# Kernel optimization log

Measured on AMD Instinct MI355X. Metric: run time of the kernel, lower is better.

Reference implementation:

```python
import jax, jax.numpy as jnp
import numpy as np

HIDDEN = [256, 128, 64, 32]
N_IN, N_OUT = 784, 10
V_REST = 0.0; V_RESET = 0.0; V_TH = 1.0; R_MEM = 1.0; DT = 1.0; TAU = 2.0
ALPHA = DT / TAU
SLOPE = 5.0
B, T = 128, 500


def setup_inputs() -> dict:
    key = jax.random.key(0)
    ks = jax.random.split(key, 7)
    sizes = [N_IN] + HIDDEN + [N_OUT]
    inp = {"input_spikes": jax.random.uniform(ks[0], (B, N_IN, T), dtype=jnp.float32)}
    for i in range(len(sizes) - 1):  # 5 weight matrices
        inp[f"w{i}"] = jax.random.uniform(ks[i + 1], (sizes[i], sizes[i + 1]), dtype=jnp.float32) * 0.1
    return inp


def _lif(v, cur):
    # voltage update, surrogate spike, hard reset (reset uses detached spike)
    v = v + (-(v - V_REST) + R_MEM * cur) * ALPHA
    s = jax.nn.sigmoid(SLOPE * (v - V_TH))
    sd = jax.lax.stop_gradient(s)
    v = v * (1.0 - sd) + V_RESET * sd
    return v, s


def reference(input_spikes, w0, w1, w2, w3, w4):
    ws = [jax.nn.relu(w) for w in (w0, w1, w2, w3, w4)]
    n_h = len(HIDDEN)
    b = input_spikes.shape[0]
    dt = input_spikes.dtype
    xs = jnp.transpose(input_spikes, (2, 0, 1))  # (T, B, N_IN)

    v0 = tuple(jnp.full((b, h), V_REST, dtype=dt) for h in HIDDEN)
    v_out0 = jnp.full((b, N_OUT), V_REST, dtype=dt)
    s_prev0 = tuple(jnp.zeros((b, h), dtype=dt) for h in HIDDEN)

    def step(carry, x_t):
        vs, v_out, s_prev = carry
        new_vs, new_s = [], []
        # layer 0 driven by current-step input
        v, s = _lif(vs[0], x_t @ ws[0])
        new_vs.append(v); new_s.append(s)
        # deeper hidden layers driven by PREVIOUS-step spikes (s_prev)
        for li in range(1, n_h):
            v, s = _lif(vs[li], s_prev[li - 1] @ ws[li])
            new_vs.append(v); new_s.append(s)
        # output layer driven by previous-step spikes of last hidden layer
        v_out, s_out = _lif(v_out, s_prev[-1] @ ws[-1])
        return (tuple(new_vs), v_out, tuple(new_s)), (tuple(new_s), s_out)

    _, (hs, outs) = jax.lax.scan(step, (v0, v_out0, s_prev0), xs)
    hidden_spikes = tuple(jnp.transpose(h, (1, 2, 0)) for h in hs)  # each (B, H, T)
    output_spikes = jnp.transpose(outs, (1, 2, 0))                   # (B, N_OUT, T)
    firing_rates = output_spikes.mean(axis=2)                         # (B, N_OUT)
    return (*hidden_spikes, output_spikes, firing_rates)
```

## Files before the change

### kernel.cpp

```cpp
#include <hip/hip_runtime.h>

#define NIN 784
#define H0 256
#define H1 128
#define H2 64
#define H3 32
#define NOUT 10
#define BATCH 128
#define TT 500
#define KCH0 25
#define JTILES 16

#define SW1 136
#define SW2 72
#define SW3 40
#define CW1 129
#define CW2 65
#define CW3 33
#define CW4 17

#define H1_OFF (BATCH * H0 * TT)
#define H2_OFF (H1_OFF + BATCH * H1 * TT)
#define H3_OFF (H2_OFF + BATCH * H2 * TT)
#define OUT_OFF (H3_OFF + BATCH * H3 * TT)
#define RATE_OFF (OUT_OFF + BATCH * NOUT * TT)

typedef __attribute__((ext_vector_type(8))) short short8v;
typedef __attribute__((ext_vector_type(4))) float f32x4;

__device__ __forceinline__ unsigned short f2bf(float f) {
  union { float f; unsigned u; } v; v.f = f;
  unsigned r = v.u + 0x7FFFu + ((v.u >> 16) & 1u);
  return (unsigned short)(r >> 16);
}
__device__ __forceinline__ float bf2f(unsigned short b) {
  union { unsigned u; float f; } v; v.u = ((unsigned)b) << 16;
  return v.f;
}

__device__ __forceinline__ float lif_step(float& v, float c) {
  v = 0.5f * (v + c);
  const float E = __expf(5.0f * (1.0f - v));
  const float r = 1.0f / (1.0f + E);
  v = v * E * r;
  return r;
}

__global__ void pack_all(const float* __restrict__ w0, const float* __restrict__ w1,
                         const float* __restrict__ w2, const float* __restrict__ w3,
                         const float* __restrict__ w4, unsigned short* __restrict__ Wf,
                         unsigned short* __restrict__ Bf) {
  const int bid = blockIdx.x, l = threadIdx.x;
  if (bid < JTILES * KCH0) {
    const int jt = bid / KCH0, kc = bid % KCH0;
    const int j = jt * 16 + (l & 15);
    const int kbase = kc * 32 + (l >> 4) * 8;
    unsigned v[4];
#pragma unroll
    for (int e = 0; e < 4; ++e) {
      const int k0 = kbase + e * 2;
      const float f0 = (k0 < NIN) ? fmaxf(w0[(size_t)k0 * H0 + j], 0.0f) : 0.0f;
      const float f1 = (k0 + 1 < NIN) ? fmaxf(w0[(size_t)(k0 + 1) * H0 + j], 0.0f) : 0.0f;
      v[e] = (unsigned)f2bf(f0) | ((unsigned)f2bf(f1) << 16);
    }
    uint4 o; o.x = v[0]; o.y = v[1]; o.z = v[2]; o.w = v[3];
    reinterpret_cast<uint4*>(Wf)[(size_t)bid * 64 + l] = o;
    return;
  }
  const int tile = bid - JTILES * KCH0;
  const float* w; int K, Nw, base, rel, KCH;
  if (tile < 64)      { w = w1; K = 256; Nw = 128; base = 0;        rel = tile;      KCH = 8; }
  else if (tile < 80) { w = w2; K = 128; Nw = 64;  base = 64 * 512; rel = tile - 64; KCH = 4; }
  else if (tile < 84) { w = w3; K = 64;  Nw = 32;  base = 80 * 512; rel = tile - 80; KCH = 2; }
  else                { w = w4; K = 32;  Nw = 10;  base = 84 * 512; rel = 0;         KCH = 1; }
  const int nt = rel / KCH, kc = rel % KCH;
  const int n = nt * 16 + (l & 15);
  const int kb = kc * 32 + (l >> 4) * 8;
  unsigned v[4];
#pragma unroll
  for (int e = 0; e < 4; ++e) {
    const int k0 = kb + e * 2;
    const float f0 = (n < Nw && k0 < K)     ? fmaxf(w[(size_t)k0 * Nw + n], 0.0f) : 0.0f;
    const float f1 = (n < Nw && k0 + 1 < K) ? fmaxf(w[(size_t)(k0 + 1) * Nw + n], 0.0f) : 0.0f;
    v[e] = (unsigned)f2bf(f0) | ((unsigned)f2bf(f1) << 16);
  }
  uint4 o; o.x = v[0]; o.y = v[1]; o.z = v[2]; o.w = v[3];
  *reinterpret_cast<uint4*>(Bf + base + ((size_t)rel * 64 + l) * 8) = o;
}

__global__ __launch_bounds__(256, 4) void gemm0(
    const float* __restrict__ X, const unsigned short* __restrict__ Wf,
    unsigned short* __restrict__ cur0) {
  const int ttile = blockIdx.x;
  const int b = blockIdx.y;
  const int tid = threadIdx.x;
  const int wave = tid >> 6, lane = tid & 63;
  const int t0 = ttile * 64;
  __shared__ unsigned short Xs[2][64 * 40];
  f32x4 acc[4][4];
#pragma unroll
  for (int i = 0; i < 4; ++i)
#pragma unroll
    for (int jj = 0; jj < 4; ++jj) acc[i][jj] = (f32x4)0.0f;

  const float* Xb = X + (size_t)b * NIN * TT;
  const int tt = tid & 63;
  const int kb = wave * 2;
  const int lrow = lane & 15, lgrp = lane >> 4;
  const int tgl = t0 + tt;
  const bool tin = tgl < TT;

  float r[8];
#pragma unroll
  for (int pp = 0; pp < 4; ++pp) {
    const int k = kb + pp * 8;
    r[pp * 2]     = tin ? Xb[(size_t)k * TT + tgl] : 0.0f;
    r[pp * 2 + 1] = tin ? Xb[(size_t)(k + 1) * TT + tgl] : 0.0f;
  }

  for (int kc = 0; kc < KCH0; ++kc) {
    unsigned short* xbuf = Xs[kc & 1];
#pragma unroll
    for (int pp = 0; pp < 4; ++pp) {
      const unsigned pk = (unsigned)f2bf(r[pp * 2]) | ((unsigned)f2bf(r[pp * 2 + 1]) << 16);
      *reinterpret_cast<unsigned*>(&xbuf[tt * 40 + kb + pp * 8]) = pk;
    }
    __syncthreads();
    if (kc + 1 < KCH0) {
      const int k0 = (kc + 1) * 32;
#pragma unroll
      for (int pp = 0; pp < 4; ++pp) {
        const int k = k0 + kb + pp * 8;
        r[pp * 2]     = (tin && k < NIN)     ? Xb[(size_t)k * TT + tgl] : 0.0f;
        r[pp * 2 + 1] = (tin && k + 1 < NIN) ? Xb[(size_t)(k + 1) * TT + tgl] : 0.0f;
      }
    }
    short8v afr[4], bfr[4];
#pragma unroll
    for (int jf = 0; jf < 4; ++jf) {
      const size_t off = ((size_t)((wave * 4 + jf) * KCH0 + kc) * 64 + lane) * 8;
      afr[jf] = *reinterpret_cast<const short8v*>(Wf + off);
    }
#pragma unroll
    for (int tf = 0; tf < 4; ++tf)
      bfr[tf] = *reinterpret_cast<const short8v*>(&xbuf[(tf * 16 + lrow) * 40 + lgrp * 8]);
#pragma unroll
    for (int jf = 0; jf < 4; ++jf)
#pragma unroll
      for (int tf = 0; tf < 4; ++tf)
        acc[jf][tf] = __builtin_amdgcn_mfma_f32_16x16x32_bf16(afr[jf], bfr[tf], acc[jf][tf], 0, 0, 0);
    __syncthreads();
  }

#pragma unroll
  for (int tf = 0; tf < 4; ++tf) {
    const int t = t0 + tf * 16 + lrow;
    if (t >= TT) continue;
    unsigned short* row = cur0 + ((size_t)b * TT + t) * H0;
#pragma unroll
    for (int jf = 0; jf < 4; ++jf) {
      const int j = wave * 64 + jf * 16 + lgrp * 4;
      const f32x4 a = acc[jf][tf];
      const unsigned p0 = (unsigned)f2bf(a[0]) | ((unsigned)f2bf(a[1]) << 16);
      const unsigned p1 = (unsigned)f2bf(a[2]) | ((unsigned)f2bf(a[3]) << 16);
      *reinterpret_cast<unsigned*>(row + j) = p0;
      *reinterpret_cast<unsigned*>(row + j + 2) = p1;
    }
  }
}

__global__ __launch_bounds__(64) void scan0(
    const unsigned short* __restrict__ cur0, unsigned short* __restrict__ s0g,
    float* __restrict__ out) {
  const int b = blockIdx.y, jg = blockIdx.x, l = threadIdx.x;
  const int j = jg * 64 + l;
  const unsigned short* cp = cur0 + (size_t)b * TT * H0 + j;
  unsigned short* sp = s0g + (size_t)b * 512 * H0 + j;
  float* hp = out + ((size_t)b * H0 + j) * TT;
  sp[0] = 0;
  float v = 0.0f;
  float c0[16], c1[16];
#define LOAD16(D, T0) _Pragma("unroll") for (int u = 0; u < 16; ++u) (D)[u] = bf2f(cp[(size_t)((T0) + u) * H0]);
#define PROC16(C, T0)                                                                \
  do {                                                                               \
    float hb[16];                                                                    \
    _Pragma("unroll")                                                                \
    for (int u = 0; u < 16; ++u) {                                                   \
      const float s = lif_step(v, (C)[u]);                                           \
      hb[u] = s;                                                                     \
      sp[(size_t)((T0) + u + 1) * H0] = f2bf(s);                                     \
    }                                                                                \
    _Pragma("unroll")                                                                \
    for (int q = 0; q < 4; ++q)                                                      \
      *reinterpret_cast<float4*>(hp + (T0) + q * 4) =                                \
          make_float4(hb[q * 4], hb[q * 4 + 1], hb[q * 4 + 2], hb[q * 4 + 3]);       \
  } while (0)
  LOAD16(c0, 0);
  for (int i = 0; i < 15; ++i) {
    const int tb = i * 32;
    LOAD16(c1, tb + 16);
    PROC16(c0, tb);
    LOAD16(c0, tb + 32);
    PROC16(c1, tb + 16);
  }
  PROC16(c0, 480);
  {
    float c[4], hb[4];
#pragma unroll
    for (int u = 0; u < 4; ++u) c[u] = bf2f(cp[(size_t)(496 + u) * H0]);
#pragma unroll
    for (int u = 0; u < 4; ++u) {
      const float s = lif_step(v, c[u]);
      hb[u] = s;
      sp[(size_t)(496 + u + 1) * H0] = f2bf(s);
    }
    *reinterpret_cast<float4*>(hp + 496) = make_float4(hb[0], hb[1], hb[2], hb[3]);
  }
#undef LOAD16
#undef PROC16
}

template<int N>
__device__ __forceinline__ void lif_dyn(float& v, float& rate, const float* cur, int cw,
                                        unsigned short* sd, int sw, float* hp, bool wsf) {
  float cr[16];
  const float* cp = cur;
#pragma unroll
  for (int u = 0; u < N; ++u) { cr[u] = *cp; cp += cw; }
  float hb[16];
  unsigned short* sp = sd;
#pragma unroll
  for (int u = 0; u < N; ++u) {
    const float s = lif_step(v, cr[u]);
    hb[u] = s;
    if (wsf) *sp = f2bf(s);
    sp += sw;
    rate += s;
  }
#pragma unroll
  for (int q = 0; q < N / 4; ++q)
    *reinterpret_cast<float4*>(hp + q * 4) =
        make_float4(hb[q * 4], hb[q * 4 + 1], hb[q * 4 + 2], hb[q * 4 + 3]);
}

__global__ __launch_bounds__(512, 1) void snn_tail14(
    const unsigned short* __restrict__ s0g, const unsigned short* __restrict__ Bf,
    float* __restrict__ out) {
  __shared__ __align__(16) unsigned short s1b[65 * SW1];
  __shared__ __align__(16) unsigned short s2b[65 * SW2];
  __shared__ __align__(16) unsigned short s3b[65 * SW3];
  __shared__ __align__(16) float c1b[64 * CW1];
  __shared__ __align__(16) float c2b[64 * CW2];
  __shared__ __align__(16) float c3b[64 * CW3];
  __shared__ __align__(16) float c4b[64 * CW4];

  const int b = blockIdx.x, tid = threadIdx.x;
  const int w = tid >> 6, lane = tid & 63, lr = lane & 15, lg = lane >> 4;
  const unsigned short* BfW1 = Bf;
  const unsigned short* BfW2 = Bf + 64 * 512;
  const unsigned short* BfW3 = Bf + 80 * 512;
  const unsigned short* BfW4 = Bf + 84 * 512;
  const unsigned short* s0b = s0g + (size_t)b * 512 * H0;

  float v = 0.0f, rate = 0.0f;
  int lay = 0, j = 0;
  const float* curb = nullptr;
  unsigned short* sb = s3b;
  float* hbase = nullptr;
  int cw = 0, sw = 0;
  bool wsf = false, sact = false;
  if (tid < 128) {
    lay = 1; j = tid; curb = c1b + j; sb = s1b; cw = CW1; sw = SW1; wsf = true;
    sact = true; hbase = out + H1_OFF + ((size_t)b * H1 + j) * TT;
  } else if (tid < 192) {
    lay = 2; j = tid - 128; curb = c2b + j; sb = s2b; cw = CW2; sw = SW2; wsf = true;
    sact = true; hbase = out + H2_OFF + ((size_t)b * H2 + j) * TT;
  } else if (tid < 224) {
    lay = 3; j = tid - 192; curb = c3b + j; sb = s3b; cw = CW3; sw = SW3; wsf = true;
    sact = true; hbase = out + H3_OFF + ((size_t)b * H3 + j) * TT;
  } else if (tid < 240) {
    lay = 4; j = tid - 224; curb = c4b + j; sb = s3b; cw = CW4; sw = 0; wsf = false;
    sact = (j < NOUT); hbase = out + OUT_OFF + ((size_t)b * NOUT + j) * TT;
  }

  for (int p = 0; p < 12; ++p) {
    if (sact) {
      const int c = p - lay;
      if (c >= 0 && c <= 7) {
        if (wsf) sb[j] = (c == 0) ? (unsigned short)0 : sb[64 * sw + j];
        float* hp = hbase + c * 64;
        unsigned short* sbj = sb + j;
        if (c < 7) {
#pragma unroll
          for (int q = 0; q < 4; ++q)
            lif_dyn<16>(v, rate, curb + q * 16 * cw, cw, sbj + (q * 16 + 1) * sw, sw,
                        hp + q * 16, wsf);
        } else {
          lif_dyn<16>(v, rate, curb, cw, sbj + 1 * sw, sw, hp, wsf);
          lif_dyn<16>(v, rate, curb + 16 * cw, cw, sbj + 17 * sw, sw, hp + 16, wsf);
          lif_dyn<16>(v, rate, curb + 32 * cw, cw, sbj + 33 * sw, sw, hp + 32, wsf);
          lif_dyn<4>(v, rate, curb + 48 * cw, cw, sbj + 49 * sw, sw, hp + 48, wsf);
        }
      }
    }
    __syncthreads();
    if (p <= 7) {
      const int tt = w >> 1, nb = (w & 1) * 4;
      short8v a[8];
      const unsigned short* ap = s0b + (size_t)(p * 64 + tt * 16 + lr) * H0 + lg * 8;
#pragma unroll
      for (int kc = 0; kc < 8; ++kc) a[kc] = *reinterpret_cast<const short8v*>(ap + kc * 32);
#pragma unroll
      for (int n4 = 0; n4 < 4; ++n4) {
        const int nt = nb + n4;
        f32x4 acc = (f32x4)0.0f;
#pragma unroll
        for (int kc = 0; kc < 8; ++kc) {
          const short8v bf = *reinterpret_cast<const short8v*>(BfW1 + ((size_t)(nt * 8 + kc) * 64 + lane) * 8);
          acc = __builtin_amdgcn_mfma_f32_16x16x32_bf16(a[kc], bf, acc, 0, 0, 0);
        }
        float* cd = c1b + (tt * 16 + lg * 4) * CW1 + nt * 16 + lr;
#pragma unroll
        for (int r = 0; r < 4; ++r) cd[r * CW1] = acc[r];
      }
    }
    if (p >= 1 && p <= 8) {
      const int tt = w >> 1;
      short8v a[4];
      const unsigned short* ap = s1b + (tt * 16 + lr) * SW1 + lg * 8;
#pragma unroll
      for (int kc = 0; kc < 4; ++kc) a[kc] = *reinterpret_cast<const short8v*>(ap + kc * 32);
#pragma unroll
      for (int qi = 0; qi < 2; ++qi) {
        const int nt = (w & 1) * 2 + qi;
        f32x4 acc = (f32x4)0.0f;
#pragma unroll
        for (int kc = 0; kc < 4; ++kc) {
          const short8v bf = *reinterpret_cast<const short8v*>(BfW2 + ((size_t)(nt * 4 + kc) * 64 + lane) * 8);
          acc = __builtin_amdgcn_mfma_f32_16x16x32_bf16(a[kc], bf, acc, 0, 0, 0);
        }
        float* cd = c2b + (tt * 16 + lg * 4) * CW2 + nt * 16 + lr;
#pragma unroll
        for (int r = 0; r < 4; ++r) cd[r * CW2] = acc[r];
      }
    }
    if (p >= 2 && p <= 9) {
      const int tt = w >> 1, nt = w & 1;
      short8v a[2];
      const unsigned short* ap = s2b + (tt * 16 + lr) * SW2 + lg * 8;
#pragma unroll
      for (int kc = 0; kc < 2; ++kc) a[kc] = *reinterpret_cast<const short8v*>(ap + kc * 32);
      f32x4 acc = (f32x4)0.0f;
#pragma unroll
      for (int kc = 0; kc < 2; ++kc) {
        const short8v bf = *reinterpret_cast<const short8v*>(BfW3 + ((size_t)(nt * 2 + kc) * 64 + lane) * 8);
        acc = __builtin_amdgcn_mfma_f32_16x16x32_bf16(a[kc], bf, acc, 0, 0, 0);
      }
      float* cd = c3b + (tt * 16 + lg * 4) * CW3 + nt * 16 + lr;
#pragma unroll
      for (int r = 0; r < 4; ++r) cd[r * CW3] = acc[r];
    }
    if (p >= 3 && p <= 10 && w < 4) {
      const int tt = w;
      const unsigned short* ap = s3b + (tt * 16 + lr) * SW3 + lg * 8;
      const short8v a0 = *reinterpret_cast<const short8v*>(ap);
      const short8v bf = *reinterpret_cast<const short8v*>(BfW4 + (size_t)lane * 8);
      f32x4 acc = (f32x4)0.0f;
      acc = __builtin_amdgcn_mfma_f32_16x16x32_bf16(a0, bf, acc, 0, 0, 0);
      float* cd = c4b + (tt * 16 + lg * 4) * CW4 + lr;
#pragma unroll
      for (int r = 0; r < 4; ++r) cd[r * CW4] = acc[r];
    }
    __syncthreads();
  }
  if (tid >= 224 && tid < 224 + NOUT)
    out[RATE_OFF + (size_t)b * NOUT + (tid - 224)] = rate * (1.0f / (float)TT);
}

extern "C" void kernel_launch(void* const* d_in, const int* in_sizes, int n_in,
                              void* d_out, int out_size, void* d_ws, size_t ws_size,
                              hipStream_t stream) {
  const float* X  = (const float*)d_in[0];
  const float* w0 = (const float*)d_in[1];
  const float* w1 = (const float*)d_in[2];
  const float* w2 = (const float*)d_in[3];
  const float* w3 = (const float*)d_in[4];
  const float* w4 = (const float*)d_in[5];
  float* out = (float*)d_out;

  uint8_t* ws = (uint8_t*)d_ws;
  const size_t SLOT = 33554432;
  unsigned short* cur0 = (unsigned short*)ws;
  unsigned short* s0g  = (unsigned short*)(ws + SLOT);
  unsigned short* Wf0  = (unsigned short*)(ws + 2 * SLOT);
  unsigned short* Bf2  = Wf0 + (size_t)JTILES * KCH0 * 64 * 8;

  pack_all<<<JTILES * KCH0 + 85, 64, 0, stream>>>(w0, w1, w2, w3, w4, Wf0, Bf2);
  gemm0<<<dim3(8, BATCH), 256, 0, stream>>>(X, Wf0, cur0);
  scan0<<<dim3(4, BATCH), 64, 0, stream>>>(cur0, s0g, out);
  snn_tail14<<<BATCH, 512, 0, stream>>>(s0g, Bf2, out);
}
```

Measured before the change: 233.4 us.

## Stage tail-kernel weights in LDS, store layer currents as bf16, prefetch layer-0 spikes

The tail kernel now copies all packed bf16 weight fragments (W1..W4) into shared memory once per block, so the MFMA B operands come from LDS rather than global memory. The per-timestep input currents for the deeper layers are stored as bf16 instead of fp32, which halves the LDS footprint needed alongside the new weight buffer, and the strides are padded to fit. The layer-0 spike A-fragments for the next chunk are loaded before the LIF phase so their global latency overlaps it. Rounding the currents to bf16 adds precision loss before the threshold, which could flip spikes near V_TH.

```diff
diff --git a/kernel.cpp b/kernel.cpp
--- a/kernel.cpp
+++ b/kernel.cpp
@@ -14,10 +14,10 @@
 #define SW1 136
 #define SW2 72
 #define SW3 40
-#define CW1 129
-#define CW2 65
-#define CW3 33
-#define CW4 17
+#define CW1 132
+#define CW2 68
+#define CW3 36
+#define CW4 20
 
 #define H1_OFF (BATCH * H0 * TT)
 #define H2_OFF (H1_OFF + BATCH * H1 * TT)
@@ -221,12 +221,13 @@
 }
 
 template<int N>
-__device__ __forceinline__ void lif_dyn(float& v, float& rate, const float* cur, int cw,
-                                        unsigned short* sd, int sw, float* hp, bool wsf) {
+__device__ __forceinline__ void lif_dynb(float& v, float& rate, const unsigned short* cur,
+                                         int cw, unsigned short* sd, int sw, float* hp,
+                                         bool wsf) {
   float cr[16];
-  const float* cp = cur;
-#pragma unroll
-  for (int u = 0; u < N; ++u) { cr[u] = *cp; cp += cw; }
+  const unsigned short* cp = cur;
+#pragma unroll
+  for (int u = 0; u < N; ++u) { cr[u] = bf2f(*cp); cp += cw; }
   float hb[16];
   unsigned short* sp = sd;
 #pragma unroll
@@ -246,25 +247,32 @@
 __global__ __launch_bounds__(512, 1) void snn_tail14(
     const unsigned short* __restrict__ s0g, const unsigned short* __restrict__ Bf,
     float* __restrict__ out) {
+  __shared__ __align__(16) unsigned short wl[85 * 512];
   __shared__ __align__(16) unsigned short s1b[65 * SW1];
   __shared__ __align__(16) unsigned short s2b[65 * SW2];
   __shared__ __align__(16) unsigned short s3b[65 * SW3];
-  __shared__ __align__(16) float c1b[64 * CW1];
-  __shared__ __align__(16) float c2b[64 * CW2];
-  __shared__ __align__(16) float c3b[64 * CW3];
-  __shared__ __align__(16) float c4b[64 * CW4];
+  __shared__ __align__(16) unsigned short c1b[64 * CW1];
+  __shared__ __align__(16) unsigned short c2b[64 * CW2];
+  __shared__ __align__(16) unsigned short c3b[64 * CW3];
+  __shared__ __align__(16) unsigned short c4b[64 * CW4];
 
   const int b = blockIdx.x, tid = threadIdx.x;
   const int w = tid >> 6, lane = tid & 63, lr = lane & 15, lg = lane >> 4;
-  const unsigned short* BfW1 = Bf;
-  const unsigned short* BfW2 = Bf + 64 * 512;
-  const unsigned short* BfW3 = Bf + 80 * 512;
-  const unsigned short* BfW4 = Bf + 84 * 512;
+  const unsigned short* WL1 = wl;
+  const unsigned short* WL2 = wl + 64 * 512;
+  const unsigned short* WL3 = wl + 80 * 512;
+  const unsigned short* WL4 = wl + 84 * 512;
   const unsigned short* s0b = s0g + (size_t)b * 512 * H0;
+
+  {
+    const uint4* src = reinterpret_cast<const uint4*>(Bf);
+    uint4* dst = reinterpret_cast<uint4*>(wl);
+    for (int i = tid; i < 85 * 512 / 8; i += 512) dst[i] = src[i];
+  }
 
   float v = 0.0f, rate = 0.0f;
   int lay = 0, j = 0;
-  const float* curb = nullptr;
+  const unsigned short* curb = nullptr;
   unsigned short* sb = s3b;
   float* hbase = nullptr;
   int cw = 0, sw = 0;
@@ -282,8 +290,16 @@
     lay = 4; j = tid - 224; curb = c4b + j; sb = s3b; cw = CW4; sw = 0; wsf = false;
     sact = (j < NOUT); hbase = out + OUT_OFF + ((size_t)b * NOUT + j) * TT;
   }
+  __syncthreads();
 
   for (int p = 0; p < 12; ++p) {
+    short8v a1[8];
+    if (p <= 7) {
+      const int tt = w >> 1;
+      const unsigned short* ap = s0b + (size_t)(p * 64 + tt * 16 + lr) * H0 + lg * 8;
+#pragma unroll
+      for (int kc = 0; kc < 8; ++kc) a1[kc] = *reinterpret_cast<const short8v*>(ap + kc * 32);
+    }
     if (sact) {
       const int c = p - lay;
       if (c >= 0 && c <= 7) {
@@ -293,35 +309,31 @@
         if (c < 7) {
 #pragma unroll
           for (int q = 0; q < 4; ++q)
-            lif_dyn<16>(v, rate, curb + q * 16 * cw, cw, sbj + (q * 16 + 1) * sw, sw,
-                        hp + q * 16, wsf);
+            lif_dynb<16>(v, rate, curb + q * 16 * cw, cw, sbj + (q * 16 + 1) * sw, sw,
+                         hp + q * 16, wsf);
         } else {
-          lif_dyn<16>(v, rate, curb, cw, sbj + 1 * sw, sw, hp, wsf);
-          lif_dyn<16>(v, rate, curb + 16 * cw, cw, sbj + 17 * sw, sw, hp + 16, wsf);
-          lif_dyn<16>(v, rate, curb + 32 * cw, cw, sbj + 33 * sw, sw, hp + 32, wsf);
-          lif_dyn<4>(v, rate, curb + 48 * cw, cw, sbj + 49 * sw, sw, hp + 48, wsf);
+          lif_dynb<16>(v, rate, curb, cw, sbj + 1 * sw, sw, hp, wsf);
+          lif_dynb<16>(v, rate, curb + 16 * cw, cw, sbj + 17 * sw, sw, hp + 16, wsf);
+          lif_dynb<16>(v, rate, curb + 32 * cw, cw, sbj + 33 * sw, sw, hp + 32, wsf);
+          lif_dynb<4>(v, rate, curb + 48 * cw, cw, sbj + 49 * sw, sw, hp + 48, wsf);
         }
       }
     }
     __syncthreads();
     if (p <= 7) {
       const int tt = w >> 1, nb = (w & 1) * 4;
-      short8v a[8];
-      const unsigned short* ap = s0b + (size_t)(p * 64 + tt * 16 + lr) * H0 + lg * 8;
-#pragma unroll
-      for (int kc = 0; kc < 8; ++kc) a[kc] = *reinterpret_cast<const short8v*>(ap + kc * 32);
 #pragma unroll
       for (int n4 = 0; n4 < 4; ++n4) {
         const int nt = nb + n4;
         f32x4 acc = (f32x4)0.0f;
 #pragma unroll
         for (int kc = 0; kc < 8; ++kc) {
-          const short8v bf = *reinterpret_cast<const short8v*>(BfW1 + ((size_t)(nt * 8 + kc) * 64 + lane) * 8);
-          acc = __builtin_amdgcn_mfma_f32_16x16x32_bf16(a[kc], bf, acc, 0, 0, 0);
+          const short8v bf = *reinterpret_cast<const short8v*>(WL1 + ((size_t)(nt * 8 + kc) * 64 + lane) * 8);
+          acc = __builtin_amdgcn_mfma_f32_16x16x32_bf16(a1[kc], bf, acc, 0, 0, 0);
         }
-        float* cd = c1b + (tt * 16 + lg * 4) * CW1 + nt * 16 + lr;
-#pragma unroll
-        for (int r = 0; r < 4; ++r) cd[r * CW1] = acc[r];
+        unsigned short* cd = c1b + (tt * 16 + lg * 4) * CW1 + nt * 16 + lr;
+#pragma unroll
+        for (int r = 0; r < 4; ++r) cd[r * CW1] = f2bf(acc[r]);
       }
     }
     if (p >= 1 && p <= 8) {
@@ -336,12 +348,12 @@
         f32x4 acc = (f32x4)0.0f;
 #pragma unroll
         for (int kc = 0; kc < 4; ++kc) {
-          const short8v bf = *reinterpret_cast<const short8v*>(BfW2 + ((size_t)(nt * 4 + kc) * 64 + lane) * 8);
+          const short8v bf = *reinterpret_cast<const short8v*>(WL2 + ((size_t)(nt * 4 + kc) * 64 + lane) * 8);
           acc = __builtin_amdgcn_mfma_f32_16x16x32_bf16(a[kc], bf, acc, 0, 0, 0);
         }
-        float* cd = c2b + (tt * 16 + lg * 4) * CW2 + nt * 16 + lr;
-#pragma unroll
-        for (int r = 0; r < 4; ++r) cd[r * CW2] = acc[r];
+        unsigned short* cd = c2b + (tt * 16 + lg * 4) * CW2 + nt * 16 + lr;
+#pragma unroll
+        for (int r = 0; r < 4; ++r) cd[r * CW2] = f2bf(acc[r]);
       }
     }
     if (p >= 2 && p <= 9) {
@@ -353,23 +365,23 @@
       f32x4 acc = (f32x4)0.0f;
 #pragma unroll
       for (int kc = 0; kc < 2; ++kc) {
-        const short8v bf = *reinterpret_cast<const short8v*>(BfW3 + ((size_t)(nt * 2 + kc) * 64 + lane) * 8);
+        const short8v bf = *reinterpret_cast<const short8v*>(WL3 + ((size_t)(nt * 2 + kc) * 64 + lane) * 8);
         acc = __builtin_amdgcn_mfma_f32_16x16x32_bf16(a[kc], bf, acc, 0, 0, 0);
       }
-      float* cd = c3b + (tt * 16 + lg * 4) * CW3 + nt * 16 + lr;
-#pragma unroll
-      for (int r = 0; r < 4; ++r) cd[r * CW3] = acc[r];
+      unsigned short* cd = c3b + (tt * 16 + lg * 4) * CW3 + nt * 16 + lr;
+#pragma unroll
+      for (int r = 0; r < 4; ++r) cd[r * CW3] = f2bf(acc[r]);
     }
     if (p >= 3 && p <= 10 && w < 4) {
       const int tt = w;
       const unsigned short* ap = s3b + (tt * 16 + lr) * SW3 + lg * 8;
       const short8v a0 = *reinterpret_cast<const short8v*>(ap);
-      const short8v bf = *reinterpret_cast<const short8v*>(BfW4 + (size_t)lane * 8);
+      const short8v bf = *reinterpret_cast<const short8v*>(WL4 + (size_t)lane * 8);
       f32x4 acc = (f32x4)0.0f;
       acc = __builtin_amdgcn_mfma_f32_16x16x32_bf16(a0, bf, acc, 0, 0, 0);
-      float* cd = c4b + (tt * 16 + lg * 4) * CW4 + lr;
-#pragma unroll
-      for (int r = 0; r < 4; ++r) cd[r * CW4] = acc[r];
+      unsigned short* cd = c4b + (tt * 16 + lg * 4) * CW4 + lr;
+#pragma unroll
+      for (int r = 0; r < 4; ++r) cd[r * CW4] = f2bf(acc[r]);
     }
     __syncthreads();
   }
```

Result: faster. 218.2 us (-6.5%).
